# Performance work log

Hardware: AMD Instinct MI355X
Metric: run time of the kernel (lower is better)

## Reference

```python
import jax, jax.numpy as jnp
import numpy as np

NIN, NHID, NDECHID, NOUT = 128, 256, 512, 10
B, N = 32, 4096


def _linear_params(key, fan_in, fan_out):
    kw, kb = jax.random.split(key)
    bound = 1.0 / np.sqrt(fan_in)
    W = jax.random.uniform(kw, (fan_in, fan_out), jnp.float32, -bound, bound)
    b = jax.random.uniform(kb, (fan_out,), jnp.float32, -bound, bound)
    return W, b


def setup_inputs() -> dict:
    key = jax.random.key(0)
    ks = jax.random.split(key, 7)
    x = jax.random.normal(ks[0], (B, N, NIN), jnp.float32)
    W1, b1 = _linear_params(ks[1], NIN, NHID)
    W2, b2 = _linear_params(ks[2], NHID, NHID)
    W3, b3 = _linear_params(ks[3], NHID, NHID)
    D1, c1 = _linear_params(ks[4], NHID, NDECHID)
    D2, c2 = _linear_params(ks[5], NDECHID, NDECHID)
    D3, c3 = _linear_params(ks[6], NDECHID, NOUT)
    return {"x": x, "W1": W1, "b1": b1, "W2": W2, "b2": b2, "W3": W3, "b3": b3,
            "D1": D1, "c1": c1, "D2": D2, "c2": c2, "D3": D3, "c3": c3}


def reference(x, W1, b1, W2, b2, W3, b3, D1, c1, D2, c2, D3, c3):
    # encoder MLP: Linear-ReLU-Linear-ReLU-Linear, then extra ReLU
    h = jax.nn.relu(x @ W1 + b1)            # [B, N, nhid]
    h = jax.nn.relu(h @ W2 + b2)
    h = jax.nn.relu(h @ W3 + b3)            # fused enc output + F.relu
    # mean_{i,j}(h_i * h_j) over the set == (mean_i h)^2 elementwise (exact identity)
    m = jnp.mean(h, axis=1)                  # [B, nhid]
    p = jax.nn.relu(m * m)                   # [B, nhid]
    # decoder MLP
    d = jax.nn.relu(p @ D1 + c1)
    d = jax.nn.relu(d @ D2 + c2)
    return d @ D3 + c3                       # [B, nout]
```

## Files before the change

### kernel.cpp

```cpp
#include <hip/hip_runtime.h>
#include <hip/hip_bf16.h>
#include <stdint.h>


#define NIN   128
#define NHID  256
#define NDEC  512
#define NOUTC 10
#define BATCH 32
#define NTOK  4096
#define MTILE 64
#define TPB   64
#define NBLK  (BATCH * TPB)
#define XPAD  136
#define HPAD  264

typedef short bf16x8 __attribute__((ext_vector_type(8)));
typedef float floatx4 __attribute__((ext_vector_type(4)));

__device__ __forceinline__ uint16_t f2b(float f) {
  union { float f; uint32_t u; } v; v.f = f;
  uint32_t r = v.u + 0x7FFFu + ((v.u >> 16) & 1u);
  return (uint16_t)(r >> 16);
}
__device__ __forceinline__ uint32_t pkbf(float lo, float hi) {
  __hip_bfloat162 h = __float22bfloat162_rn(float2{lo, hi});
  union { __hip_bfloat162 h; uint32_t u; } c; c.h = h;
  return c.u;
}

__global__ __launch_bounds__(256) void pack_weights(
    const float* __restrict__ W1, const float* __restrict__ W2,
    const float* __restrict__ W3, uint16_t* __restrict__ out,
    float* __restrict__ msum) {
  int p = blockIdx.x * blockDim.x + threadIdx.x;
  if (p < BATCH * NHID) msum[p] = 0.f;
  const float* W; int K; int base;
  if (p < 32768)      { W = W1; K = NIN;  base = 0; }
  else if (p < 98304) { W = W2; K = NHID; base = 32768; p -= 32768; }
  else                { W = W3; K = NHID; base = 98304; p -= 98304; }
  int j    = p & 7;
  int lane = (p >> 3) & 63;
  int rest = p >> 9;
  int KC = K >> 5;
  int kc = rest % KC;
  int mt = rest / KC;
  int m = mt * 16 + (lane & 15);
  int k = kc * 32 + ((lane >> 4) << 3) + j;
  out[base + (((mt * KC + kc) * 64 + lane) << 3) + j] = f2b(W[k * NHID + m]);
}

__global__ __launch_bounds__(256) void encoder(
    const float* __restrict__ x,
    const uint16_t* __restrict__ pW,
    const float* __restrict__ b1,
    const float* __restrict__ b2,
    const float* __restrict__ b3,
    float* __restrict__ msum) {
  __shared__ uint16_t Hs[MTILE * HPAD];

  const int tid  = threadIdx.x;
  const int wave = tid >> 6;
  const int lane = tid & 63;
  const int l15  = lane & 15;
  const int q    = lane >> 4;
  const int tok0 = blockIdx.x * MTILE;

  const uint16_t* pW1 = pW;
  const uint16_t* pW2 = pW + 32768;
  const uint16_t* pW3 = pW + 98304;

  {
    const int row = tid >> 2;
    const int c0  = (tid & 3) * 32;
    const float* xr = x + (size_t)(tok0 + row) * NIN + c0;
    for (int i = 0; i < 8; ++i) {
      float4 v = *(const float4*)(xr + i * 4);
      uint2 u = make_uint2(pkbf(v.x, v.y), pkbf(v.z, v.w));
      *(uint2*)&Hs[row * XPAD + c0 + i * 4] = u;
    }
  }
  __syncthreads();

  floatx4 acc[4][4];

  for (int jt = 0; jt < 4; ++jt)
    for (int tt = 0; tt < 4; ++tt)
      acc[jt][tt] = (floatx4){0.f, 0.f, 0.f, 0.f};
#pragma unroll
  for (int kc = 0; kc < 4; ++kc) {
    bf16x8 a[4], b[4];
#pragma unroll
    for (int jt = 0; jt < 4; ++jt)
      a[jt] = *(const bf16x8*)(pW1 + ((((wave * 4 + jt) * 4 + kc) * 64 + lane) << 3));
#pragma unroll
    for (int tt = 0; tt < 4; ++tt)
      b[tt] = *(const bf16x8*)&Hs[(tt * 16 + l15) * XPAD + kc * 32 + q * 8];
#pragma unroll
    for (int jt = 0; jt < 4; ++jt)
#pragma unroll
      for (int tt = 0; tt < 4; ++tt)
        acc[jt][tt] = __builtin_amdgcn_mfma_f32_16x16x32_bf16(
            a[jt], b[tt], acc[jt][tt], 0, 0, 0);
  }
  __syncthreads();

#pragma unroll
  for (int jt = 0; jt < 4; ++jt) {
    const int jbase = wave * 64 + jt * 16 + q * 4;
    const float4 bb = *(const float4*)&b1[jbase];
#pragma unroll
    for (int tt = 0; tt < 4; ++tt) {
      const int t = tt * 16 + l15;
      float v0 = fmaxf(acc[jt][tt][0] + bb.x, 0.f);
      float v1 = fmaxf(acc[jt][tt][1] + bb.y, 0.f);
      float v2 = fmaxf(acc[jt][tt][2] + bb.z, 0.f);
      float v3 = fmaxf(acc[jt][tt][3] + bb.w, 0.f);
      *(uint2*)&Hs[t * HPAD + jbase] = make_uint2(pkbf(v0, v1), pkbf(v2, v3));
    }
  }
  __syncthreads();

  for (int jt = 0; jt < 4; ++jt)
    for (int tt = 0; tt < 4; ++tt)
      acc[jt][tt] = (floatx4){0.f, 0.f, 0.f, 0.f};
#pragma unroll
  for (int kc = 0; kc < 8; ++kc) {
    bf16x8 a[4], b[4];
#pragma unroll
    for (int jt = 0; jt < 4; ++jt)
      a[jt] = *(const bf16x8*)(pW2 + ((((wave * 4 + jt) * 8 + kc) * 64 + lane) << 3));
#pragma unroll
    for (int tt = 0; tt < 4; ++tt)
      b[tt] = *(const bf16x8*)&Hs[(tt * 16 + l15) * HPAD + kc * 32 + q * 8];
#pragma unroll
    for (int jt = 0; jt < 4; ++jt)
#pragma unroll
      for (int tt = 0; tt < 4; ++tt)
        acc[jt][tt] = __builtin_amdgcn_mfma_f32_16x16x32_bf16(
            a[jt], b[tt], acc[jt][tt], 0, 0, 0);
  }
  __syncthreads();
#pragma unroll
  for (int jt = 0; jt < 4; ++jt) {
    const int jbase = wave * 64 + jt * 16 + q * 4;
    const float4 bb = *(const float4*)&b2[jbase];
#pragma unroll
    for (int tt = 0; tt < 4; ++tt) {
      const int t = tt * 16 + l15;
      float v0 = fmaxf(acc[jt][tt][0] + bb.x, 0.f);
      float v1 = fmaxf(acc[jt][tt][1] + bb.y, 0.f);
      float v2 = fmaxf(acc[jt][tt][2] + bb.z, 0.f);
      float v3 = fmaxf(acc[jt][tt][3] + bb.w, 0.f);
      *(uint2*)&Hs[t * HPAD + jbase] = make_uint2(pkbf(v0, v1), pkbf(v2, v3));
    }
  }
  __syncthreads();

  for (int jt = 0; jt < 4; ++jt)
    for (int tt = 0; tt < 4; ++tt)
      acc[jt][tt] = (floatx4){0.f, 0.f, 0.f, 0.f};
#pragma unroll
  for (int kc = 0; kc < 8; ++kc) {
    bf16x8 a[4], b[4];
#pragma unroll
    for (int jt = 0; jt < 4; ++jt)
      a[jt] = *(const bf16x8*)(pW3 + ((((wave * 4 + jt) * 8 + kc) * 64 + lane) << 3));
#pragma unroll
    for (int tt = 0; tt < 4; ++tt)
      b[tt] = *(const bf16x8*)&Hs[(tt * 16 + l15) * HPAD + kc * 32 + q * 8];
#pragma unroll
    for (int jt = 0; jt < 4; ++jt)
#pragma unroll
      for (int tt = 0; tt < 4; ++tt)
        acc[jt][tt] = __builtin_amdgcn_mfma_f32_16x16x32_bf16(
            a[jt], b[tt], acc[jt][tt], 0, 0, 0);
  }
  __syncthreads();

  {
    float4* scratch = (float4*)Hs;
#pragma unroll
    for (int jt = 0; jt < 4; ++jt) {
      const int jbase = wave * 64 + jt * 16 + q * 4;
      const float4 bb = *(const float4*)&b3[jbase];
      float s0 = 0.f, s1 = 0.f, s2 = 0.f, s3 = 0.f;
#pragma unroll
      for (int tt = 0; tt < 4; ++tt) {
        s0 += fmaxf(acc[jt][tt][0] + bb.x, 0.f);
        s1 += fmaxf(acc[jt][tt][1] + bb.y, 0.f);
        s2 += fmaxf(acc[jt][tt][2] + bb.z, 0.f);
        s3 += fmaxf(acc[jt][tt][3] + bb.w, 0.f);
      }
      scratch[((wave * 4 + jt) * 4 + q) * 17 + l15] =
          (float4){s0, s1, s2, s3};
    }
  }
  __syncthreads();
  {
    const int c = tid >> 2;
    const int r = tid & 3;
    const float* sf = (const float*)Hs;
    float v = 0.f;
#pragma unroll
    for (int l = 0; l < 16; ++l)
      v += sf[c * 68 + l * 4 + r];
    const int wv = c >> 4, jt = (c >> 2) & 3, qq = c & 3;
    const int j = wv * 64 + jt * 16 + qq * 4 + r;
    const int batch = blockIdx.x >> 6;
    atomicAdd(&msum[batch * NHID + j], v);
  }
}

__global__ __launch_bounds__(1024) void decoder(
    const float* __restrict__ msum,
    const float* __restrict__ D1, const float* __restrict__ c1,
    const float* __restrict__ D2, const float* __restrict__ c2,
    const float* __restrict__ D3, const float* __restrict__ c3,
    float* __restrict__ out) {
  __shared__ float p[NHID];
  __shared__ float d1[NDEC];
  __shared__ float d2[NDEC];
  __shared__ float red[1024];
  const int b = blockIdx.x, t = threadIdx.x;

  if (t < NHID) {
    float m = msum[b * NHID + t] * (1.f / NTOK);
    p[t] = m * m;
  }
  __syncthreads();

  const int j = t & 511;
  const int h = t >> 9;

  {
    float s = 0.f;
    for (int k = h * 128; k < h * 128 + 128; ++k)
      s += p[k] * D1[k * NDEC + j];
    red[t] = s;
    __syncthreads();
    if (t < NDEC)
      d1[t] = fmaxf(red[t] + red[512 + t] + c1[t], 0.f);
    __syncthreads();
  }

  {
    float s = 0.f;
    for (int k = h * 256; k < h * 256 + 256; ++k)
      s += d1[k] * D2[k * NDEC + j];
    red[t] = s;
    __syncthreads();
    if (t < NDEC)
      d2[t] = fmaxf(red[t] + red[512 + t] + c2[t], 0.f);
    __syncthreads();
  }

  {
    const int j3 = t & 15;
    const int kc = t >> 4;
    float s = 0.f;
    if (j3 < NOUTC)
      for (int k = kc * 8; k < kc * 8 + 8; ++k)
        s += d2[k] * D3[k * NOUTC + j3];
    red[t] = s;
    __syncthreads();
    if (t < NOUTC) {
      float v = c3[t];
#pragma unroll
      for (int i = 0; i < 64; ++i) v += red[i * 16 + t];
      out[b * NOUTC + t] = v;
    }
  }
}

extern "C" void kernel_launch(void* const* d_in, const int* in_sizes, int n_in,
                              void* d_out, int out_size, void* d_ws, size_t ws_size,
                              hipStream_t stream) {
  const float* x  = (const float*)d_in[0];
  const float* W1 = (const float*)d_in[1];
  const float* b1 = (const float*)d_in[2];
  const float* W2 = (const float*)d_in[3];
  const float* b2 = (const float*)d_in[4];
  const float* W3 = (const float*)d_in[5];
  const float* b3 = (const float*)d_in[6];
  const float* D1 = (const float*)d_in[7];
  const float* c1 = (const float*)d_in[8];
  const float* D2 = (const float*)d_in[9];
  const float* c2 = (const float*)d_in[10];
  const float* D3 = (const float*)d_in[11];
  const float* c3 = (const float*)d_in[12];

  uint16_t* pW   = (uint16_t*)d_ws;
  float*    msum = (float*)((char*)d_ws + 384 * 1024);

  pack_weights<<<640, 256, 0, stream>>>(W1, W2, W3, pW, msum);
  encoder<<<NBLK, 256, 0, stream>>>(x, pW, b1, b2, b3, msum);
  decoder<<<BATCH, 1024, 0, stream>>>(msum, D1, c1, D2, c2, D3, c3,
                                      (float*)d_out);
}
```

Baseline: 176.4 us.

## Fuse pack, encoder and decoder into one cooperative persistent kernel

Replaces the three kernel launches with a single cooperative kernel that packs the weights, runs the encoder tiles in a persistent grid-stride loop, and runs the decoder layers, with grid.sync between phases. The decoder is also split across 256 blocks (batch x output chunk) instead of 32 blocks, so more CUs share the D1/D2 reads. The aim is to remove launch gaps and the serial tail of the 32-block decoder. In exchange it adds grid-wide barrier costs and caps the encoder grid at what can be co-resident, and it falls back to the old three-launch path if the cooperative launch fails.

```diff
diff --git a/kernel.cpp b/kernel.cpp
--- a/kernel.cpp
+++ b/kernel.cpp
@@ -1,6 +1,9 @@
 #include <hip/hip_runtime.h>
+#include <hip/hip_cooperative_groups.h>
 #include <hip/hip_bf16.h>
 #include <stdint.h>
+
+namespace cg = cooperative_groups;
 
 
 #define NIN   128
@@ -10,8 +13,7 @@
 #define BATCH 32
 #define NTOK  4096
 #define MTILE 64
-#define TPB   64
-#define NBLK  (BATCH * TPB)
+#define NBLK  (BATCH * (NTOK / MTILE))
 #define XPAD  136
 #define HPAD  264
 
@@ -19,7 +21,7 @@
 typedef float floatx4 __attribute__((ext_vector_type(4)));
 
 __device__ __forceinline__ uint16_t f2b(float f) {
-  union { float f; uint32_t u; } v; v.f = f;
+  union { uint32_t u; float f; } v; v.f = f;
   uint32_t r = v.u + 0x7FFFu + ((v.u >> 16) & 1u);
   return (uint16_t)(r >> 16);
 }
@@ -29,42 +31,35 @@
   return c.u;
 }
 
-__global__ __launch_bounds__(256) void pack_weights(
-    const float* __restrict__ W1, const float* __restrict__ W2,
-    const float* __restrict__ W3, uint16_t* __restrict__ out,
-    float* __restrict__ msum) {
-  int p = blockIdx.x * blockDim.x + threadIdx.x;
-  if (p < BATCH * NHID) msum[p] = 0.f;
+__device__ __forceinline__ void pack_one(
+    int p, const float* __restrict__ W1, const float* __restrict__ W2,
+    const float* __restrict__ W3, uint16_t* __restrict__ pW) {
   const float* W; int K; int base;
   if (p < 32768)      { W = W1; K = NIN;  base = 0; }
   else if (p < 98304) { W = W2; K = NHID; base = 32768; p -= 32768; }
   else                { W = W3; K = NHID; base = 98304; p -= 98304; }
   int j    = p & 7;
-  int lane = (p >> 3) & 63;
+  int ln   = (p >> 3) & 63;
   int rest = p >> 9;
   int KC = K >> 5;
   int kc = rest % KC;
   int mt = rest / KC;
-  int m = mt * 16 + (lane & 15);
-  int k = kc * 32 + ((lane >> 4) << 3) + j;
-  out[base + (((mt * KC + kc) * 64 + lane) << 3) + j] = f2b(W[k * NHID + m]);
-}
-
-__global__ __launch_bounds__(256) void encoder(
-    const float* __restrict__ x,
-    const uint16_t* __restrict__ pW,
-    const float* __restrict__ b1,
-    const float* __restrict__ b2,
-    const float* __restrict__ b3,
-    float* __restrict__ msum) {
-  __shared__ uint16_t Hs[MTILE * HPAD];
-
-  const int tid  = threadIdx.x;
+  int m = mt * 16 + (ln & 15);
+  int k = kc * 32 + ((ln >> 4) << 3) + j;
+  pW[base + (((mt * KC + kc) * 64 + ln) << 3) + j] = f2b(W[k * NHID + m]);
+}
+
+__device__ __forceinline__ void encoder_tile(
+    int tile, int tid, uint16_t* Hs,
+    const float* __restrict__ x, const uint16_t* __restrict__ pW,
+    const float* __restrict__ b1, const float* __restrict__ b2,
+    const float* __restrict__ b3, float* __restrict__ msum) {
   const int wave = tid >> 6;
   const int lane = tid & 63;
   const int l15  = lane & 15;
   const int q    = lane >> 4;
-  const int tok0 = blockIdx.x * MTILE;
+  const int tok0  = tile * MTILE;
+  const int batch = tile >> 6;
 
   const uint16_t* pW1 = pW;
   const uint16_t* pW2 = pW + 32768;
@@ -192,8 +187,7 @@
         s2 += fmaxf(acc[jt][tt][2] + bb.z, 0.f);
         s3 += fmaxf(acc[jt][tt][3] + bb.w, 0.f);
       }
-      scratch[((wave * 4 + jt) * 4 + q) * 17 + l15] =
-          (float4){s0, s1, s2, s3};
+      scratch[((wave * 4 + jt) * 4 + q) * 17 + l15] = (float4){s0, s1, s2, s3};
     }
   }
   __syncthreads();
@@ -207,9 +201,130 @@
       v += sf[c * 68 + l * 4 + r];
     const int wv = c >> 4, jt = (c >> 2) & 3, qq = c & 3;
     const int j = wv * 64 + jt * 16 + qq * 4 + r;
-    const int batch = blockIdx.x >> 6;
     atomicAdd(&msum[batch * NHID + j], v);
   }
+}
+
+__global__ __launch_bounds__(256) void fused(
+    const float* __restrict__ x,
+    const float* __restrict__ W1, const float* __restrict__ b1,
+    const float* __restrict__ W2, const float* __restrict__ b2,
+    const float* __restrict__ W3, const float* __restrict__ b3,
+    const float* __restrict__ D1, const float* __restrict__ c1,
+    const float* __restrict__ D2, const float* __restrict__ c2,
+    const float* __restrict__ D3, const float* __restrict__ c3,
+    uint16_t* __restrict__ pW, float* __restrict__ msum,
+    float* __restrict__ d1s, float* __restrict__ d2s,
+    float* __restrict__ out) {
+  cg::grid_group grid = cg::this_grid();
+  __shared__ __align__(16) uint16_t Hs[MTILE * HPAD];
+
+  const int tid = threadIdx.x;
+  const int gstep = gridDim.x * 256;
+
+  for (int p0 = blockIdx.x * 256 + tid; p0 < 163840; p0 += gstep)
+    pack_one(p0, W1, W2, W3, pW);
+  for (int p0 = blockIdx.x * 256 + tid; p0 < BATCH * NHID; p0 += gstep)
+    msum[p0] = 0.f;
+  __threadfence();
+  grid.sync();
+
+  for (int tile = blockIdx.x; tile < NBLK; tile += gridDim.x) {
+    __syncthreads();
+    encoder_tile(tile, tid, Hs, x, pW, b1, b2, b3, msum);
+  }
+  __threadfence();
+  grid.sync();
+
+  for (int blk = blockIdx.x; blk < 256; blk += gridDim.x) {
+    const int b = blk >> 3, jc = blk & 7;
+    float* p   = (float*)Hs;
+    float* red = p + 256;
+    __syncthreads();
+    {
+      float m = msum[b * NHID + tid] * (1.f / NTOK);
+      p[tid] = m * m;
+    }
+    __syncthreads();
+    const int j  = jc * 64 + (tid & 63);
+    const int kc = tid >> 6;
+    float s = 0.f;
+    for (int k = kc * 64; k < kc * 64 + 64; ++k)
+      s += p[k] * D1[k * NDEC + j];
+    red[tid] = s;
+    __syncthreads();
+    if (tid < 64) {
+      float v = red[tid] + red[64 + tid] + red[128 + tid] + red[192 + tid]
+              + c1[jc * 64 + tid];
+      d1s[b * NDEC + jc * 64 + tid] = fmaxf(v, 0.f);
+    }
+  }
+  __threadfence();
+  grid.sync();
+
+  for (int blk = blockIdx.x; blk < 256; blk += gridDim.x) {
+    const int b = blk >> 3, jc = blk & 7;
+    float* h   = (float*)Hs;
+    float* red = h + NDEC;
+    __syncthreads();
+    h[tid]       = d1s[b * NDEC + tid];
+    h[tid + 256] = d1s[b * NDEC + tid + 256];
+    __syncthreads();
+    const int j  = jc * 64 + (tid & 63);
+    const int kc = tid >> 6;
+    float s = 0.f;
+    for (int k = kc * 128; k < kc * 128 + 128; ++k)
+      s += h[k] * D2[k * NDEC + j];
+    red[tid] = s;
+    __syncthreads();
+    if (tid < 64) {
+      float v = red[tid] + red[64 + tid] + red[128 + tid] + red[192 + tid]
+              + c2[jc * 64 + tid];
+      d2s[b * NDEC + jc * 64 + tid] = fmaxf(v, 0.f);
+    }
+  }
+  __threadfence();
+  grid.sync();
+
+  for (int blk = blockIdx.x; blk < BATCH; blk += gridDim.x) {
+    float* h   = (float*)Hs;
+    float* red = h + NDEC;
+    __syncthreads();
+    h[tid]       = d2s[blk * NDEC + tid];
+    h[tid + 256] = d2s[blk * NDEC + tid + 256];
+    __syncthreads();
+    const int j3 = tid & 15;
+    const int kc = tid >> 4;
+    float s = 0.f;
+    if (j3 < NOUTC)
+      for (int k = kc * 32; k < kc * 32 + 32; ++k)
+        s += h[k] * D3[k * NOUTC + j3];
+    red[tid] = s;
+    __syncthreads();
+    if (tid < NOUTC) {
+      float v = c3[tid];
+#pragma unroll
+      for (int i = 0; i < 16; ++i) v += red[i * 16 + tid];
+      out[blk * NOUTC + tid] = v;
+    }
+  }
+}
+
+__global__ __launch_bounds__(256) void pack_weights(
+    const float* __restrict__ W1, const float* __restrict__ W2,
+    const float* __restrict__ W3, uint16_t* __restrict__ pW,
+    float* __restrict__ msum) {
+  int p = blockIdx.x * blockDim.x + threadIdx.x;
+  if (p < BATCH * NHID) msum[p] = 0.f;
+  pack_one(p, W1, W2, W3, pW);
+}
+
+__global__ __launch_bounds__(256) void encoder(
+    const float* __restrict__ x, const uint16_t* __restrict__ pW,
+    const float* __restrict__ b1, const float* __restrict__ b2,
+    const float* __restrict__ b3, float* __restrict__ msum) {
+  __shared__ __align__(16) uint16_t Hs[MTILE * HPAD];
+  encoder_tile(blockIdx.x, threadIdx.x, Hs, x, pW, b1, b2, b3, msum);
 }
 
 __global__ __launch_bounds__(1024) void decoder(
@@ -243,7 +358,6 @@
       d1[t] = fmaxf(red[t] + red[512 + t] + c1[t], 0.f);
     __syncthreads();
   }
-
   {
     float s = 0.f;
     for (int k = h * 256; k < h * 256 + 256; ++k)
@@ -254,7 +368,6 @@
       d2[t] = fmaxf(red[t] + red[512 + t] + c2[t], 0.f);
     __syncthreads();
   }
-
   {
     const int j3 = t & 15;
     const int kc = t >> 4;
@@ -272,6 +385,8 @@
     }
   }
 }
+
+static int g_coop_failed = 0;
 
 extern "C" void kernel_launch(void* const* d_in, const int* in_sizes, int n_in,
                               void* d_out, int out_size, void* d_ws, size_t ws_size,
@@ -292,9 +407,37 @@
 
   uint16_t* pW   = (uint16_t*)d_ws;
   float*    msum = (float*)((char*)d_ws + 384 * 1024);
+  float*    d1s  = (float*)((char*)d_ws + 448 * 1024);
+  float*    d2s  = (float*)((char*)d_ws + 512 * 1024);
+  float*    out  = (float*)d_out;
+
+  if (!g_coop_failed) {
+    int dev = 0;
+    (void)hipGetDevice(&dev);
+    int mp = 0;
+    if (hipDeviceGetAttribute(&mp, hipDeviceAttributeMultiprocessorCount,
+                              dev) != hipSuccess || mp <= 0)
+      mp = 256;
+    int nb = 0;
+    if (hipOccupancyMaxActiveBlocksPerMultiprocessor(
+            &nb, (const void*)fused, 256, 0) != hipSuccess || nb < 1)
+      nb = 1;
+    long grid = (long)nb * (long)mp;
+    if (grid > NBLK) grid = NBLK;
+    if (grid < 1) grid = 1;
+
+    void* args[] = {
+        (void*)&x,  (void*)&W1, (void*)&b1, (void*)&W2, (void*)&b2,
+        (void*)&W3, (void*)&b3, (void*)&D1, (void*)&c1, (void*)&D2,
+        (void*)&c2, (void*)&D3, (void*)&c3, (void*)&pW, (void*)&msum,
+        (void*)&d1s, (void*)&d2s, (void*)&out};
+    hipError_t e = hipLaunchCooperativeKernel(
+        (const void*)fused, dim3((unsigned)grid), dim3(256), args, 0, stream);
+    if (e == hipSuccess) return;
+    g_coop_failed = 1;
+  }
 
   pack_weights<<<640, 256, 0, stream>>>(W1, W2, W3, pW, msum);
   encoder<<<NBLK, 256, 0, stream>>>(x, pW, b1, b2, b3, msum);
-  decoder<<<BATCH, 1024, 0, stream>>>(msum, D1, c1, D2, c2, D3, c3,
-                                      (float*)d_out);
-}
+  decoder<<<BATCH, 1024, 0, stream>>>(msum, D1, c1, D2, c2, D3, c3, out);
+}
```

New measurement: 176.3 us. Within noise of the previous version (-0.0%).
